# Kernel tuning notes

Hardware: AMD Instinct MI355X
Metric: run time of the kernel (lower is better)

## Reference

```python
import jax, jax.numpy as jnp
import numpy as np

WINDOW_SIZE = 11
SIGMA = 1.5
C1 = 0.01 ** 2
C2 = 0.03 ** 2


def _gaussian_window(window_size, sigma, channel):
    xs = np.arange(window_size)
    g = np.exp(-((xs - window_size // 2) ** 2) / (2.0 * sigma ** 2))
    g = (g / g.sum()).astype(np.float32)
    w2d = np.outer(g, g)  # [k,k]
    # depthwise kernel layout OIHW with O=channel, I=1
    return jnp.asarray(np.broadcast_to(w2d, (channel, 1, window_size, window_size)).copy())


def _blur(x, window, channel):
    # depthwise conv, SAME-style padding = k//2 (k odd -> exact SAME)
    pad = WINDOW_SIZE // 2
    return jax.lax.conv_general_dilated(
        x, window,
        window_strides=(1, 1),
        padding=[(pad, pad), (pad, pad)],
        dimension_numbers=('NCHW', 'OIHW', 'NCHW'),
        feature_group_count=channel,
    )


def setup_inputs() -> dict:
    key = jax.random.key(0)
    k1, k2 = jax.random.split(key)
    shape = (32, 3, 512, 512)
    img1 = jax.random.uniform(k1, shape, dtype=jnp.float32)
    img2 = jax.random.uniform(k2, shape, dtype=jnp.float32)
    return {"img1": img1, "img2": img2}


def reference(img1, img2):
    channel = img1.shape[1]
    window = _gaussian_window(WINDOW_SIZE, SIGMA, channel).astype(img1.dtype)

    mu1 = _blur(img1, window, channel)
    mu2 = _blur(img2, window, channel)
    mu1_sq = mu1 * mu1
    mu2_sq = mu2 * mu2
    mu1_mu2 = mu1 * mu2

    sigma1_sq = _blur(img1 * img1, window, channel) - mu1_sq
    sigma2_sq = _blur(img2 * img2, window, channel) - mu2_sq
    sigma12 = _blur(img1 * img2, window, channel) - mu1_mu2

    ssim_map = ((2 * mu1_mu2 + C1) * (2 * sigma12 + C2)) / (
        (mu1_sq + mu2_sq + C1) * (sigma1_sq + sigma2_sq + C2))
    return 1.0 - jnp.mean(ssim_map)
```

## Files before the change

### kernel.cpp

```cpp
#include <hip/hip_runtime.h>


#define HH 512
#define WW 512
#define TILE 32
#define IN_ROWS 42
#define RADX 8
#define SQUADS 12
#define S_STRIDE 50
#define H_STRIDE 33
#define NPLANES 96
#define NPIX 25165824.0f
#define NACC 256

#define H01_OFF 0
#define H23_OFF 11088
#define H4_OFF  22176
#define UNION_BYTES 27720

typedef float v2f __attribute__((ext_vector_type(2)));
typedef float v4f __attribute__((ext_vector_type(4)));

__global__ __launch_bounds__(256, 5) void ssim_fused_kernel(
    const float* __restrict__ img1, const float* __restrict__ img2,
    float* __restrict__ acc) {
  __shared__ __align__(16) char ubuf[UNION_BYTES];
  __shared__ float wsum[4];

  v2f (*s12)[S_STRIDE] = (v2f (*)[S_STRIDE])ubuf;
  v2f (*h01)[H_STRIDE] = (v2f (*)[H_STRIDE])(ubuf + H01_OFF);
  v2f (*h23)[H_STRIDE] = (v2f (*)[H_STRIDE])(ubuf + H23_OFF);
  float (*h4)[H_STRIDE] = (float (*)[H_STRIDE])(ubuf + H4_OFF);

  const int tid = threadIdx.x;
  const int tx = blockIdx.x * TILE;
  const int ty = blockIdx.y * TILE;
  const size_t base = (size_t)blockIdx.z * (HH * WW);

  const float g[11] = {
      1.0283800e-03f, 7.5987600e-03f, 3.6000770e-02f, 1.0936072e-01f,
      2.1300560e-01f, 2.6601170e-01f, 2.1300560e-01f, 1.0936072e-01f,
      3.6000770e-02f, 7.5987600e-03f, 1.0283800e-03f};

#pragma unroll
  for (int it = 0; it < 2; ++it) {
    int idx = it * 256 + tid;
    if (idx < IN_ROWS * SQUADS) {
      int r = idx / SQUADS;
      int p = idx - r * SQUADS;
      int gy = ty - 5 + r;
      int gx = tx - RADX + 4 * p;
      v4f A = {0.f, 0.f, 0.f, 0.f}, B = {0.f, 0.f, 0.f, 0.f};
      if ((unsigned)gy < (unsigned)HH && (unsigned)gx < (unsigned)WW) {
        size_t off = base + (size_t)gy * WW + gx;
        A = *(const v4f*)(img1 + off);
        B = *(const v4f*)(img2 + off);
      }
      *(v4f*)&s12[r][4 * p]     = (v4f){A.x, B.x, A.y, B.y};
      *(v4f*)&s12[r][4 * p + 2] = (v4f){A.z, B.z, A.w, B.w};
    }
  }
  __syncthreads();

  v2f p01[6], p23[6];
  float p4[6];
#pragma unroll
  for (int it = 0; it < 6; ++it) {
    int idx = it * 256 + tid;
    if (idx < IN_ROWS * TILE) {
      int r = idx >> 5;
      int c = idx & 31;
      v2f a01 = (v2f){0.f, 0.f};
      v2f a23 = (v2f){0.f, 0.f};
      float a4 = 0.f;
#pragma unroll
      for (int dx = 0; dx < 11; ++dx) {
        v2f v = s12[r][c + dx + 3];
        float w = g[dx];
        a01 += w * v;
        v2f sq = v * v;
        a23 += w * sq;
        a4 = __builtin_fmaf(w, v.x * v.y, a4);
      }
      p01[it] = a01;
      p23[it] = a23;
      p4[it] = a4;
    }
  }
  __syncthreads();

#pragma unroll
  for (int it = 0; it < 6; ++it) {
    int idx = it * 256 + tid;
    if (idx < IN_ROWS * TILE) {
      int r = idx >> 5;
      int c = idx & 31;
      h01[r][c] = p01[it];
      h23[r][c] = p23[it];
      h4[r][c] = p4[it];
    }
  }
  __syncthreads();

  const float C1 = 1e-4f;
  const float C2 = 9e-4f;
  const int c = tid & 31;
  const int r0 = (tid >> 5) * 4;

  v2f m[4], vv[4];
  float b12[4];
#pragma unroll
  for (int o = 0; o < 4; ++o) {
    m[o] = (v2f){0.f, 0.f};
    vv[o] = (v2f){0.f, 0.f};
    b12[o] = 0.f;
  }

#pragma unroll
  for (int dy = 0; dy < 14; ++dy) {
    v2f a = h01[r0 + dy][c];
    v2f b = h23[r0 + dy][c];
    float d = h4[r0 + dy][c];
#pragma unroll
    for (int o = 0; o < 4; ++o) {
      const int k = dy - o;
      if (k >= 0 && k < 11) {
        float w = g[k];
        m[o] += w * a;
        vv[o] += w * b;
        b12[o] = __builtin_fmaf(w, d, b12[o]);
      }
    }
  }

  float lsum = 0.f;
#pragma unroll
  for (int o = 0; o < 4; ++o) {
    float mu1 = m[o].x, mu2 = m[o].y;
    float mu1sq = mu1 * mu1;
    float mu2sq = mu2 * mu2;
    float mu12 = mu1 * mu2;
    float sig11 = vv[o].x - mu1sq;
    float sig22 = vv[o].y - mu2sq;
    float sig12 = b12[o] - mu12;
    float num = (2.f * mu12 + C1) * (2.f * sig12 + C2);
    float den = (mu1sq + mu2sq + C1) * (sig11 + sig22 + C2);
    lsum += num * __builtin_amdgcn_rcpf(den);
  }

#pragma unroll
  for (int off = 32; off > 0; off >>= 1)
    lsum += __shfl_down(lsum, off, 64);
  const int lane = tid & 63;
  const int wid = tid >> 6;
  if (lane == 0) wsum[wid] = lsum;
  __syncthreads();
  if (tid == 0) {
    float b = wsum[0] + wsum[1] + wsum[2] + wsum[3];
    int slot = (blockIdx.x + blockIdx.y * 16 + blockIdx.z) & (NACC - 1);
    atomicAdd(acc + slot, b);
  }
}

__global__ void ssim_finalize_kernel(const float* __restrict__ acc,
                                     float* __restrict__ out) {
  __shared__ float wsum[4];
  const int tid = threadIdx.x;
  float s = acc[tid];
#pragma unroll
  for (int off = 32; off > 0; off >>= 1)
    s += __shfl_down(s, off, 64);
  if ((tid & 63) == 0) wsum[tid >> 6] = s;
  __syncthreads();
  if (tid == 0)
    out[0] = 1.0f - (wsum[0] + wsum[1] + wsum[2] + wsum[3]) * (1.0f / NPIX);
}

extern "C" void kernel_launch(void* const* d_in, const int* in_sizes, int n_in,
                              void* d_out, int out_size, void* d_ws, size_t ws_size,
                              hipStream_t stream) {
  const float* img1 = (const float*)d_in[0];
  const float* img2 = (const float*)d_in[1];
  float* out = (float*)d_out;
  float* acc = (float*)d_ws;

  hipMemsetAsync(acc, 0, NACC * sizeof(float), stream);

  dim3 grid(WW / TILE, HH / TILE, NPLANES);
  ssim_fused_kernel<<<grid, 256, 0, stream>>>(img1, img2, acc);
  ssim_finalize_kernel<<<1, NACC, 0, stream>>>(acc, out);
}
```

Before: 287.8 us.

## Switch separable Gaussian blur to packed fp16 with dot2 instructions

Inputs are converted to packed fp16 and the squared and cross products are precomputed in fp16, then stored as five planes in shared memory. Both the horizontal and vertical passes now use v_dot2 fp16 instructions with precomputed weight pairs, and the intermediate is stored transposed in fp16. This roughly halves LDS footprint and ALU instruction count and allows higher occupancy (launch bounds raised to 7). The trade-off is reduced precision: fp16 rounding of x^2 and of blur sums followed by variance subtraction can perturb the SSIM result.

```diff
diff --git a/kernel.cpp b/kernel.cpp
--- a/kernel.cpp
+++ b/kernel.cpp
@@ -5,144 +5,172 @@
 #define WW 512
 #define TILE 32
 #define IN_ROWS 42
-#define RADX 8
-#define SQUADS 12
-#define S_STRIDE 50
-#define H_STRIDE 33
+#define SDW 26
+#define AQ_BYTES (IN_ROWS * SDW * 4)
+#define HDW 23
+#define HQ_BYTES (TILE * HDW * 4)
+#define UNION_BYTES (5 * AQ_BYTES)
 #define NPLANES 96
 #define NPIX 25165824.0f
 #define NACC 256
 
-#define H01_OFF 0
-#define H23_OFF 11088
-#define H4_OFF  22176
-#define UNION_BYTES 27720
-
-typedef float v2f __attribute__((ext_vector_type(2)));
+#define G0 1.0283800e-03f
+#define G1 7.5987600e-03f
+#define G2 3.6000770e-02f
+#define G3 1.0936072e-01f
+#define G4 2.1300560e-01f
+#define G5 2.6601170e-01f
+#define G6 2.1300560e-01f
+#define G7 1.0936072e-01f
+#define G8 3.6000770e-02f
+#define G9 7.5987600e-03f
+#define G10 1.0283800e-03f
+
 typedef float v4f __attribute__((ext_vector_type(4)));
-
-__global__ __launch_bounds__(256, 5) void ssim_fused_kernel(
+typedef __fp16 h2 __attribute__((ext_vector_type(2)));
+
+#define H2C(a, b) ((h2){(__fp16)(a), (__fp16)(b)})
+
+static __device__ __forceinline__ unsigned bc(h2 v) {
+  return __builtin_bit_cast(unsigned, v);
+}
+static __device__ __forceinline__ h2 bh(unsigned u) {
+  return __builtin_bit_cast(h2, u);
+}
+static __device__ __forceinline__ float dot2(unsigned d, h2 w, float s) {
+  return __builtin_amdgcn_fdot2(bh(d), w, s, false);
+}
+
+__global__ __launch_bounds__(256, 7) void ssim_fused_kernel(
     const float* __restrict__ img1, const float* __restrict__ img2,
     float* __restrict__ acc) {
-  __shared__ __align__(16) char ubuf[UNION_BYTES];
+  __shared__ __align__(16) char ub[UNION_BYTES];
   __shared__ float wsum[4];
-
-  v2f (*s12)[S_STRIDE] = (v2f (*)[S_STRIDE])ubuf;
-  v2f (*h01)[H_STRIDE] = (v2f (*)[H_STRIDE])(ubuf + H01_OFF);
-  v2f (*h23)[H_STRIDE] = (v2f (*)[H_STRIDE])(ubuf + H23_OFF);
-  float (*h4)[H_STRIDE] = (float (*)[H_STRIDE])(ubuf + H4_OFF);
 
   const int tid = threadIdx.x;
   const int tx = blockIdx.x * TILE;
   const int ty = blockIdx.y * TILE;
   const size_t base = (size_t)blockIdx.z * (HH * WW);
 
-  const float g[11] = {
-      1.0283800e-03f, 7.5987600e-03f, 3.6000770e-02f, 1.0936072e-01f,
-      2.1300560e-01f, 2.6601170e-01f, 2.1300560e-01f, 1.0936072e-01f,
-      3.6000770e-02f, 7.5987600e-03f, 1.0283800e-03f};
-
 #pragma unroll
   for (int it = 0; it < 2; ++it) {
     int idx = it * 256 + tid;
-    if (idx < IN_ROWS * SQUADS) {
-      int r = idx / SQUADS;
-      int p = idx - r * SQUADS;
+    if (idx < IN_ROWS * 12) {
+      int r = idx / 12;
+      int p = idx - r * 12;
       int gy = ty - 5 + r;
-      int gx = tx - RADX + 4 * p;
+      int gx = tx - 8 + 4 * p;
       v4f A = {0.f, 0.f, 0.f, 0.f}, B = {0.f, 0.f, 0.f, 0.f};
       if ((unsigned)gy < (unsigned)HH && (unsigned)gx < (unsigned)WW) {
         size_t off = base + (size_t)gy * WW + gx;
         A = *(const v4f*)(img1 + off);
         B = *(const v4f*)(img2 + off);
       }
-      *(v4f*)&s12[r][4 * p]     = (v4f){A.x, B.x, A.y, B.y};
-      *(v4f*)&s12[r][4 * p + 2] = (v4f){A.z, B.z, A.w, B.w};
+      h2 x1a = __builtin_amdgcn_cvt_pkrtz(A.x, A.y);
+      h2 x1b = __builtin_amdgcn_cvt_pkrtz(A.z, A.w);
+      h2 x2a = __builtin_amdgcn_cvt_pkrtz(B.x, B.y);
+      h2 x2b = __builtin_amdgcn_cvt_pkrtz(B.z, B.w);
+      h2 s1a = x1a * x1a, s1b = x1b * x1b;
+      h2 s2a = x2a * x2a, s2b = x2b * x2b;
+      h2 xya = x1a * x2a, xyb = x1b * x2b;
+      char* wp = ub + (r * SDW + 2 * p) * 4;
+      *(uint2*)(wp + 0 * AQ_BYTES) = make_uint2(bc(x1a), bc(x1b));
+      *(uint2*)(wp + 1 * AQ_BYTES) = make_uint2(bc(x2a), bc(x2b));
+      *(uint2*)(wp + 2 * AQ_BYTES) = make_uint2(bc(s1a), bc(s1b));
+      *(uint2*)(wp + 3 * AQ_BYTES) = make_uint2(bc(s2a), bc(s2b));
+      *(uint2*)(wp + 4 * AQ_BYTES) = make_uint2(bc(xya), bc(xyb));
     }
   }
   __syncthreads();
 
-  v2f p01[6], p23[6];
-  float p4[6];
+  const int c = tid & 31;
+  const int w = tid >> 5;
+  const int k0 = (c + 3) >> 1;
+  const bool codd = (c & 1) != 0;
+  const h2 wp0 = codd ? H2C(G0, G1) : H2C(0.f, G0);
+  const h2 wp1 = codd ? H2C(G2, G3) : H2C(G1, G2);
+  const h2 wp2 = codd ? H2C(G4, G5) : H2C(G3, G4);
+  const h2 wp3 = codd ? H2C(G6, G7) : H2C(G5, G6);
+  const h2 wp4 = codd ? H2C(G8, G9) : H2C(G7, G8);
+  const h2 wp5 = codd ? H2C(G10, 0.f) : H2C(G9, G10);
+
+  float res[6][5];
 #pragma unroll
   for (int it = 0; it < 6; ++it) {
-    int idx = it * 256 + tid;
-    if (idx < IN_ROWS * TILE) {
-      int r = idx >> 5;
-      int c = idx & 31;
-      v2f a01 = (v2f){0.f, 0.f};
-      v2f a23 = (v2f){0.f, 0.f};
-      float a4 = 0.f;
-#pragma unroll
-      for (int dx = 0; dx < 11; ++dx) {
-        v2f v = s12[r][c + dx + 3];
-        float w = g[dx];
-        a01 += w * v;
-        v2f sq = v * v;
-        a23 += w * sq;
-        a4 = __builtin_fmaf(w, v.x * v.y, a4);
+    int r = it * 8 + w;
+    if (r < IN_ROWS) {
+      const char* ap = ub + (r * SDW + k0) * 4;
+#pragma unroll
+      for (int q = 0; q < 5; ++q) {
+        const unsigned* dp = (const unsigned*)(ap + q * AQ_BYTES);
+        float s = 0.f;
+        s = dot2(dp[0], wp0, s);
+        s = dot2(dp[1], wp1, s);
+        s = dot2(dp[2], wp2, s);
+        s = dot2(dp[3], wp3, s);
+        s = dot2(dp[4], wp4, s);
+        s = dot2(dp[5], wp5, s);
+        res[it][q] = s;
       }
-      p01[it] = a01;
-      p23[it] = a23;
-      p4[it] = a4;
     }
   }
   __syncthreads();
 
+  __fp16* hb = (__fp16*)ub;
 #pragma unroll
   for (int it = 0; it < 6; ++it) {
-    int idx = it * 256 + tid;
-    if (idx < IN_ROWS * TILE) {
-      int r = idx >> 5;
-      int c = idx & 31;
-      h01[r][c] = p01[it];
-      h23[r][c] = p23[it];
-      h4[r][c] = p4[it];
+    int r = it * 8 + w;
+    if (r < IN_ROWS) {
+#pragma unroll
+      for (int q = 0; q < 5; ++q)
+        hb[q * (HQ_BYTES / 2) + c * (HDW * 2) + r] = (__fp16)res[it][q];
     }
   }
   __syncthreads();
+
+  const char* hp = ub + c * (HDW * 4) + w * 8;
+  float accq[5][4];
+#pragma unroll
+  for (int q = 0; q < 5; ++q) {
+    const unsigned* dp = (const unsigned*)(hp + q * HQ_BYTES);
+    unsigned d0 = dp[0], d1 = dp[1], d2 = dp[2], d3 = dp[3];
+    unsigned d4 = dp[4], d5 = dp[5], d6 = dp[6];
+    float s;
+    s = 0.f;
+    s = dot2(d0, H2C(G0, G1), s);  s = dot2(d1, H2C(G2, G3), s);
+    s = dot2(d2, H2C(G4, G5), s);  s = dot2(d3, H2C(G6, G7), s);
+    s = dot2(d4, H2C(G8, G9), s);  s = dot2(d5, H2C(G10, 0.f), s);
+    accq[q][0] = s;
+    s = 0.f;
+    s = dot2(d0, H2C(0.f, G0), s); s = dot2(d1, H2C(G1, G2), s);
+    s = dot2(d2, H2C(G3, G4), s);  s = dot2(d3, H2C(G5, G6), s);
+    s = dot2(d4, H2C(G7, G8), s);  s = dot2(d5, H2C(G9, G10), s);
+    accq[q][1] = s;
+    s = 0.f;
+    s = dot2(d1, H2C(G0, G1), s);  s = dot2(d2, H2C(G2, G3), s);
+    s = dot2(d3, H2C(G4, G5), s);  s = dot2(d4, H2C(G6, G7), s);
+    s = dot2(d5, H2C(G8, G9), s);  s = dot2(d6, H2C(G10, 0.f), s);
+    accq[q][2] = s;
+    s = 0.f;
+    s = dot2(d1, H2C(0.f, G0), s); s = dot2(d2, H2C(G1, G2), s);
+    s = dot2(d3, H2C(G3, G4), s);  s = dot2(d4, H2C(G5, G6), s);
+    s = dot2(d5, H2C(G7, G8), s);  s = dot2(d6, H2C(G9, G10), s);
+    accq[q][3] = s;
+  }
 
   const float C1 = 1e-4f;
   const float C2 = 9e-4f;
-  const int c = tid & 31;
-  const int r0 = (tid >> 5) * 4;
-
-  v2f m[4], vv[4];
-  float b12[4];
+  float lsum = 0.f;
 #pragma unroll
   for (int o = 0; o < 4; ++o) {
-    m[o] = (v2f){0.f, 0.f};
-    vv[o] = (v2f){0.f, 0.f};
-    b12[o] = 0.f;
-  }
-
-#pragma unroll
-  for (int dy = 0; dy < 14; ++dy) {
-    v2f a = h01[r0 + dy][c];
-    v2f b = h23[r0 + dy][c];
-    float d = h4[r0 + dy][c];
-#pragma unroll
-    for (int o = 0; o < 4; ++o) {
-      const int k = dy - o;
-      if (k >= 0 && k < 11) {
-        float w = g[k];
-        m[o] += w * a;
-        vv[o] += w * b;
-        b12[o] = __builtin_fmaf(w, d, b12[o]);
-      }
-    }
-  }
-
-  float lsum = 0.f;
-#pragma unroll
-  for (int o = 0; o < 4; ++o) {
-    float mu1 = m[o].x, mu2 = m[o].y;
+    float mu1 = accq[0][o], mu2 = accq[1][o];
+    float b11 = accq[2][o], b22 = accq[3][o], b12 = accq[4][o];
     float mu1sq = mu1 * mu1;
     float mu2sq = mu2 * mu2;
     float mu12 = mu1 * mu2;
-    float sig11 = vv[o].x - mu1sq;
-    float sig22 = vv[o].y - mu2sq;
-    float sig12 = b12[o] - mu12;
+    float sig11 = b11 - mu1sq;
+    float sig22 = b22 - mu2sq;
+    float sig12 = b12 - mu12;
     float num = (2.f * mu12 + C1) * (2.f * sig12 + C2);
     float den = (mu1sq + mu2sq + C1) * (sig11 + sig22 + C2);
     lsum += num * __builtin_amdgcn_rcpf(den);
@@ -184,7 +212,7 @@
   float* out = (float*)d_out;
   float* acc = (float*)d_ws;
 
-  hipMemsetAsync(acc, 0, NACC * sizeof(float), stream);
+  (void)hipMemsetAsync(acc, 0, NACC * sizeof(float), stream);
 
   dim3 grid(WW / TILE, HH / TILE, NPLANES);
   ssim_fused_kernel<<<grid, 256, 0, stream>>>(img1, img2, acc);
```

Result: slower. 403.3 us (+40.1%).
